# Kernel optimization log

Hardware: AMD Instinct MI355X
Metric: run time of the kernel (lower is better)

Reference implementation:

```python
import jax, jax.numpy as jnp
import numpy as np

B, S, H = 4, 2048, 512
DEPTH, EXP = 2, 4
MAX_LR = 0.1
C = 8            # n_chunks
L = S // C       # chunk length
HE = H * EXP


def _l2norm(x, eps=1e-12):
    n = jnp.sqrt(jnp.sum(x * x, axis=-1, keepdims=True))
    return x / jnp.maximum(n, eps)


def _mem_fwd(mw1, mb1, mw2, mb2, x):
    # ResLinear: residual MLP blocks, x <- x + W2 @ silu(W1 @ x + b1) + b2
    for d in range(DEPTH):
        h = jax.nn.silu(x @ mw1[d].T + mb1[d])
        x = x + h @ mw2[d].T + mb2[d]
    return x


def setup_inputs() -> dict:
    key = jax.random.key(0)
    ks = jax.random.split(key, 9)
    s = 1.0 / np.sqrt(H)
    s2 = 1.0 / np.sqrt(HE)
    return {
        "x": jax.random.normal(ks[0], (B, S, H), jnp.float32),
        "wq": jax.random.normal(ks[1], (H, H), jnp.float32) * s, "bq": jnp.zeros((H,), jnp.float32),
        "wk": jax.random.normal(ks[2], (H, H), jnp.float32) * s, "bk": jnp.zeros((H,), jnp.float32),
        "wv": jax.random.normal(ks[3], (H, H), jnp.float32) * s, "bv": jnp.zeros((H,), jnp.float32),
        "wlr": jax.random.normal(ks[4], (1, H), jnp.float32) * s, "blr": jnp.zeros((1,), jnp.float32),
        "wf": jax.random.normal(ks[5], (1, H), jnp.float32) * s, "bf": jnp.zeros((1,), jnp.float32),
        "wm": jax.random.normal(ks[6], (1, H), jnp.float32) * s, "bm": jnp.zeros((1,), jnp.float32),
        "mw1": jax.random.normal(ks[7], (DEPTH, HE, H), jnp.float32) * s,
        "mb1": jnp.zeros((DEPTH, HE), jnp.float32),
        "mw2": jax.random.normal(ks[8], (DEPTH, H, HE), jnp.float32) * s2,
        "mb2": jnp.zeros((DEPTH, H), jnp.float32),
        "mom_w1": jnp.zeros((DEPTH, HE, H), jnp.float32),
        "mom_b1": jnp.zeros((DEPTH, HE), jnp.float32),
        "mom_w2": jnp.zeros((DEPTH, H, HE), jnp.float32),
        "mom_b2": jnp.zeros((DEPTH, H), jnp.float32),
    }


def reference(x, wq, bq, wk, bk, wv, bv, wlr, blr, wf, bf, wm, bm,
              mw1, mb1, mw2, mb2, mom_w1, mom_b1, mom_w2, mom_b2):
    # projections (non-generating path; S % C == 0 so no padding)
    q = _l2norm(x @ wq.T + bq)                            # [B,S,H]
    k = _l2norm(x @ wk.T + bk).reshape(B, C, L, H)
    v = (x @ wv.T + bv).reshape(B, C, L, H)
    lr = jax.nn.sigmoid(x @ wlr.T + blr).reshape(B, C, L, 1) * MAX_LR
    forget = jax.nn.sigmoid(x @ wf.T + bf).reshape(B, C, L, 1)
    momg = jax.nn.sigmoid(x @ wm.T + bm).reshape(B, C, L, 1)

    mem = (mw1, mb1, mw2, mb2)

    def chunk_loss(mem_params, k_c, v_c, lr_c):
        # k_c,v_c: [B,L,H]; lr_c: [B,L,1]
        preds = _mem_fwd(*mem_params, k_c)
        loss = jnp.mean((preds - v_c) ** 2, axis=-1)      # [B,L]
        return jnp.sum(loss * lr_c[..., 0])

    # per-chunk synthetic gradients of the memory MLP, then mean over chunks
    grads = jax.vmap(jax.grad(chunk_loss), in_axes=(None, 1, 1, 1))(mem, k, v, lr)
    grads = jax.tree_util.tree_map(lambda g: jnp.mean(g, axis=0), grads)

    alpha = jnp.mean(forget, axis=(1, 2, 3))              # [B] forget gate
    theta = jnp.mean(lr, axis=(1, 2, 3))                  # [B] adaptive lr
    eta = jnp.mean(momg, axis=(1, 2, 3))                  # [B] momentum gate

    def update(p, g, m):
        shp = (B,) + (1,) * p.ndim
        a, t, e = alpha.reshape(shp), theta.reshape(shp), eta.reshape(shp)
        m_b = e * m[None] - t * g[None]                   # [B,*p.shape]
        return jnp.mean(p[None] * (1.0 - a) + m_b, axis=0)

    moms = (mom_w1, mom_b1, mom_w2, mom_b2)
    new_mem = tuple(update(p, g, m) for p, g, m in zip(mem, grads, moms))

    return _mem_fwd(*new_mem, q)                          # [B,S,H]
```

## Files before the change

### kernel.cpp

```cpp
#include <hip/hip_runtime.h>
#include <cstdint>
#include <cstddef>


#define NROWS 8192
#define HDIM  512
#define HEDIM 2048
#define NCHUNK 8
#define BK    64
#define DPCOEF (2.0f / (HDIM * NCHUNK))

typedef unsigned short u16;
typedef __attribute__((ext_vector_type(8))) unsigned short u16x8;
typedef __attribute__((ext_vector_type(8))) short bf16x8;
typedef __attribute__((ext_vector_type(4))) float f32x4;

__device__ __forceinline__ float sigmoidf_(float x){ return 1.0f/(1.0f+__expf(-x)); }
__device__ __forceinline__ float siluf_(float x){ return x*sigmoidf_(x); }
__device__ __forceinline__ float dsiluf_(float x){ float s=sigmoidf_(x); return s*(1.0f+x*(1.0f-s)); }
__device__ __forceinline__ u16 bf1_(float x){
    union{float f; unsigned u;} v; v.f = x;
    return (u16)((v.u + 0x7fffu + ((v.u>>16)&1u)) >> 16);
}
__device__ __forceinline__ float bf2f_(u16 h){
    union{unsigned u; float f;} v; v.u = ((unsigned)h) << 16; return v.f;
}
__device__ __forceinline__ int swkey_(int row){
    return (((row>>3)&1)<<2) | (((row>>4)&1)<<1) | ((row>>5)&1);
}
__device__ __forceinline__ void gl_lds16(const u16* g, u16* l){
    __builtin_amdgcn_global_load_lds(
        (const __attribute__((address_space(1))) unsigned*)g,
        (__attribute__((address_space(3))) unsigned*)l, 16, 0, 0);
}

template<int MODE, bool ATR>
__global__ __launch_bounds__(256)
void mgemm_k(const u16* __restrict__ A, const u16* __restrict__ B,
             const float* __restrict__ bias, const float* __restrict__ resF,
             const u16* __restrict__ resB, const u16* __restrict__ aux,
             const float* __restrict__ vf, const float* __restrict__ lrs,
             float* __restrict__ outF, u16* __restrict__ outB, u16* __restrict__ outB2,
             int M, int N, int K, int lda, int ldb)
{
    __shared__ __align__(128) u16 As[128*64];
    __shared__ __align__(128) u16 Bs[128*64];
    const int tid = threadIdx.x;
    const int lane = tid & 63, wvi = tid >> 6;
    const int wm = wvi >> 1, wn = wvi & 1;
    const int lr = lane & 15, lq = lane >> 4;
    const int m0 = blockIdx.y * 128, n0 = blockIdx.x * 128;

    int kbeg = 0, kend = K;
    if (MODE == 3){ const int ks = K >> 3; kbeg = blockIdx.z * ks; kend = kbeg + ks; }

    f32x4 acc[4][4];
    const f32x4 zz = {0.f,0.f,0.f,0.f};
    #pragma unroll
    for (int i = 0; i < 4; ++i)
        #pragma unroll
        for (int j = 0; j < 4; ++j) acc[i][j] = zz;

    int roffA[4], roffB[4];
    #pragma unroll
    for (int i = 0; i < 4; ++i){
        const int ra = wm*64 + i*16 + lr, rb = wn*64 + i*16 + lr;
        roffA[i] = ra*64 + ((lq ^ swkey_(ra)) << 3);
        roffB[i] = rb*64 + ((lq ^ swkey_(rb)) << 3);
    }

    for (int k0 = kbeg; k0 < kend; k0 += BK) {
        if (!ATR) {
            #pragma unroll
            for (int it = 0; it < 4; ++it){
                const int seg = it*4 + wvi;
                const int key = (((seg&1)<<2)|(((seg>>1)&1)<<1)|((seg>>2)&1));
                const int row = seg*8 + (lane>>3);
                const int chunk = (lane&7) ^ key;
                gl_lds16(A + (size_t)(m0+row)*lda + k0 + chunk*8, &As[seg*512]);
                gl_lds16(B + (size_t)(n0+row)*ldb + k0 + chunk*8, &Bs[seg*512]);
            }
        } else {
            #pragma unroll
            for (int r = 0; r < 2; ++r){
                const int slot = r*256 + tid;
                const int mc = slot & 15, kp = slot >> 4;
                const int chunk = kp >> 2, t = kp & 3;
                const int key = (((mc&1)<<2)|(((mc>>1)&1)<<1)|((mc>>2)&1));
                const int cs = ((chunk ^ key) << 3) + t*2;
                {
                    const u16* p = A + (size_t)(k0 + 2*kp) * lda + m0 + mc*8;
                    u16x8 e = *(const u16x8*)p;
                    u16x8 o = *(const u16x8*)(p + lda);
                    #pragma unroll
                    for (int j = 0; j < 8; ++j)
                        *(unsigned*)&As[(mc*8 + j)*64 + cs] = (unsigned)e[j] | ((unsigned)o[j] << 16);
                }
                {
                    const u16* p = B + (size_t)(k0 + 2*kp) * ldb + n0 + mc*8;
                    u16x8 e = *(const u16x8*)p;
                    u16x8 o = *(const u16x8*)(p + ldb);
                    #pragma unroll
                    for (int j = 0; j < 8; ++j)
                        *(unsigned*)&Bs[(mc*8 + j)*64 + cs] = (unsigned)e[j] | ((unsigned)o[j] << 16);
                }
            }
        }
        __syncthreads();
        #pragma unroll
        for (int ks = 0; ks < 2; ++ks) {
            bf16x8 afr[4], bfr[4];
            #pragma unroll
            for (int i = 0; i < 4; ++i){
                const int ra = wm*64 + i*16 + lr, rb = wn*64 + i*16 + lr;
                afr[i] = *(const bf16x8*)&As[ra*64 + (((ks*4 + lq) ^ swkey_(ra)) << 3)];
                bfr[i] = *(const bf16x8*)&Bs[rb*64 + (((ks*4 + lq) ^ swkey_(rb)) << 3)];
            }
            #pragma unroll
            for (int mi = 0; mi < 4; ++mi)
                #pragma unroll
                for (int ni = 0; ni < 4; ++ni)
                    acc[mi][ni] = __builtin_amdgcn_mfma_f32_16x16x32_bf16(afr[mi], bfr[ni], acc[mi][ni], 0, 0, 0);
        }
        __syncthreads();
    }
    (void)roffA; (void)roffB;

    #pragma unroll
    for (int ni = 0; ni < 4; ++ni){
        const int col = n0 + wn*64 + ni*16 + lr;
        float bv = 0.0f;
        if (MODE==0 || MODE==1 || MODE==2 || MODE==6 || MODE==7 || MODE==8 || MODE==9) bv = bias[col];
        #pragma unroll
        for (int mi = 0; mi < 4; ++mi){
            const int rbase = m0 + wm*64 + mi*16 + lq*4;
            #pragma unroll
            for (int v = 0; v < 4; ++v){
                const int row = rbase + v;
                const size_t idx = (size_t)row * N + col;
                const float o = acc[mi][ni][v];
                if (MODE == 0){ outF[idx] = o + bv; }
                else if (MODE == 1){
                    const float u = o + bv;
                    outB[idx]  = bf1_(siluf_(u));
                    outB2[idx] = bf1_(dsiluf_(u));
                }
                else if (MODE == 2){ outB[idx] = bf1_(siluf_(o + bv)); }
                else if (MODE == 3){ outF[(size_t)blockIdx.z * M * N + idx] = o; }
                else if (MODE == 4){ outB[idx] = bf1_(o * bf2f_(aux[idx])); }
                else if (MODE == 5){ outB[idx] = bf1_(o + resF[idx]); }
                else if (MODE == 6){ const float t = o + bv + resF[idx]; outF[idx] = t; outB[idx] = bf1_(t); }
                else if (MODE == 7){ outF[idx] = o + bv + resF[idx]; }
                else if (MODE == 8){
                    const float t = o + bv + bf2f_(resB[idx]);
                    const float g = lrs[row] * DPCOEF * (t - vf[idx]);
                    outF[idx] = g; outB[idx] = bf1_(g);
                }
                else if (MODE == 9){ outB[idx] = bf1_(o + bv + bf2f_(resB[idx])); }
            }
        }
    }
}

__global__ __launch_bounds__(256)
void cvt_k(const float* __restrict__ in, u16* __restrict__ out, int n8)
{
    const int i = blockIdx.x * 256 + threadIdx.x;
    if (i < n8){
        const float4 a = *(const float4*)(in + (size_t)i*8);
        const float4 b = *(const float4*)(in + (size_t)i*8 + 4);
        u16x8 o;
        o[0]=bf1_(a.x); o[1]=bf1_(a.y); o[2]=bf1_(a.z); o[3]=bf1_(a.w);
        o[4]=bf1_(b.x); o[5]=bf1_(b.y); o[6]=bf1_(b.z); o[7]=bf1_(b.w);
        *(u16x8*)(out + (size_t)i*8) = o;
    }
}

__global__ __launch_bounds__(256)
void tcvt_k(const float* __restrict__ in, u16* __restrict__ out, int R, int C)
{
    __shared__ float t[32][33];
    const int tx = threadIdx.x & 31, ty = threadIdx.x >> 5;
    const int c0 = blockIdx.x * 32, r0 = blockIdx.y * 32;
    #pragma unroll
    for (int j = 0; j < 4; ++j)
        t[ty + 8*j][tx] = in[(size_t)(r0 + ty + 8*j) * C + c0 + tx];
    __syncthreads();
    #pragma unroll
    for (int j = 0; j < 4; ++j)
        out[(size_t)(c0 + ty + 8*j) * R + r0 + tx] = bf1_(t[tx][ty + 8*j]);
}

template<bool WF32>
__global__ __launch_bounds__(64)
void l2norm_k(const float* __restrict__ in, float* __restrict__ outF, u16* __restrict__ outB)
{
    const float* p = in + (size_t)blockIdx.x * HDIM;
    const int t = threadIdx.x;
    float4 v0 = *(const float4*)(p + t*8), v1 = *(const float4*)(p + t*8 + 4);
    float s = v0.x*v0.x+v0.y*v0.y+v0.z*v0.z+v0.w*v0.w
            + v1.x*v1.x+v1.y*v1.y+v1.z*v1.z+v1.w*v1.w;
    #pragma unroll
    for (int o = 1; o < 64; o <<= 1) s += __shfl_xor(s, o);
    const float sc = 1.0f / fmaxf(sqrtf(s), 1e-12f);
    v0.x*=sc; v0.y*=sc; v0.z*=sc; v0.w*=sc;
    v1.x*=sc; v1.y*=sc; v1.z*=sc; v1.w*=sc;
    if (WF32){
        float* q = outF + (size_t)blockIdx.x * HDIM;
        *(float4*)(q + t*8) = v0; *(float4*)(q + t*8 + 4) = v1;
    }
    u16x8 ob;
    ob[0]=bf1_(v0.x); ob[1]=bf1_(v0.y); ob[2]=bf1_(v0.z); ob[3]=bf1_(v0.w);
    ob[4]=bf1_(v1.x); ob[5]=bf1_(v1.y); ob[6]=bf1_(v1.z); ob[7]=bf1_(v1.w);
    *(u16x8*)(outB + (size_t)blockIdx.x * HDIM + t*8) = ob;
}

__global__ __launch_bounds__(64)
void gates_k(const float* __restrict__ x,
             const float* __restrict__ wlr, const float* __restrict__ blr,
             const float* __restrict__ wf,  const float* __restrict__ bfp,
             const float* __restrict__ wm,  const float* __restrict__ bm,
             float* __restrict__ lr_s, float* __restrict__ f_s, float* __restrict__ m_s)
{
    const size_t row = blockIdx.x;
    const float* p = x + row * HDIM;
    const int t = threadIdx.x;
    float s0 = 0.f, s1 = 0.f, s2 = 0.f;
    #pragma unroll
    for (int i = 0; i < 8; i += 4){
        float4 xv = *(const float4*)(p   + t*8 + i);
        float4 a  = *(const float4*)(wlr + t*8 + i);
        float4 b  = *(const float4*)(wf  + t*8 + i);
        float4 c  = *(const float4*)(wm  + t*8 + i);
        s0 += xv.x*a.x + xv.y*a.y + xv.z*a.z + xv.w*a.w;
        s1 += xv.x*b.x + xv.y*b.y + xv.z*b.z + xv.w*b.w;
        s2 += xv.x*c.x + xv.y*c.y + xv.z*c.z + xv.w*c.w;
    }
    #pragma unroll
    for (int o = 1; o < 64; o <<= 1){
        s0 += __shfl_xor(s0, o); s1 += __shfl_xor(s1, o); s2 += __shfl_xor(s2, o);
    }
    if (t == 0){
        lr_s[row] = sigmoidf_(s0 + blr[0]) * 0.1f;
        f_s[row]  = sigmoidf_(s1 + bfp[0]);
        m_s[row]  = sigmoidf_(s2 + bm[0]);
    }
}

__global__ __launch_bounds__(256)
void scalars_k(const float* __restrict__ lr_s, const float* __restrict__ f_s,
               const float* __restrict__ m_s, float* __restrict__ sc)
{
    __shared__ float sh0[256], sh1[256], sh2[256];
    const int t = threadIdx.x;
    float s0 = 0.f, s1 = 0.f, s2 = 0.f;
    for (int i = t; i < NROWS; i += 256){ s0 += f_s[i]; s1 += lr_s[i]; s2 += m_s[i]; }
    sh0[t] = s0; sh1[t] = s1; sh2[t] = s2;
    __syncthreads();
    for (int o = 128; o > 0; o >>= 1){
        if (t < o){ sh0[t] += sh0[t+o]; sh1[t] += sh1[t+o]; sh2[t] += sh2[t+o]; }
        __syncthreads();
    }
    if (t == 0){
        sc[0] = sh0[0] / (float)NROWS;
        sc[1] = sh1[0] / (float)NROWS;
        sc[2] = sh2[0] / (float)NROWS;
    }
}

template<typename T>
__global__ __launch_bounds__(64)
void colsum_part_k(const T* __restrict__ g, float* __restrict__ part, int cols)
{
    const int c = blockIdx.x * 64 + threadIdx.x;
    const int rc = blockIdx.y;
    const T* p = g + (size_t)rc * 128 * cols + c;
    float s = 0.f;
    for (int r = 0; r < 128; ++r){
        if (sizeof(T) == 2) s += bf2f_(*(const u16*)(p + (size_t)r * cols));
        else                s += *(const float*)(p + (size_t)r * cols);
    }
    part[(size_t)rc * cols + c] = s;
}
__global__ __launch_bounds__(256)
void colsum_fin_k(const float* __restrict__ part, float* __restrict__ out, int cols)
{
    const int c = blockIdx.x * 256 + threadIdx.x;
    if (c < cols){
        float s = 0.f;
        for (int r = 0; r < 64; ++r) s += part[(size_t)r * cols + c];
        out[c] = s;
    }
}

__global__ __launch_bounds__(256)
void update_k(const float* __restrict__ p, const float* __restrict__ g,
              const float* __restrict__ mom, const float* __restrict__ sc,
              float* __restrict__ np_, int n)
{
    const int i = blockIdx.x * 256 + threadIdx.x;
    if (i < n) np_[i] = p[i] * (1.0f - sc[0]) + sc[2] * mom[i] - sc[1] * g[i];
}

__global__ __launch_bounds__(256)
void fupdate8_k(const float* __restrict__ p, const float* __restrict__ P,
                const float* __restrict__ mom, const float* __restrict__ sc,
                u16* __restrict__ nWb, int n)
{
    const int i = blockIdx.x * 256 + threadIdx.x;
    if (i < n){
        float g = 0.f;
        #pragma unroll
        for (int z = 0; z < 8; ++z) g += P[(size_t)z * n + i];
        nWb[i] = bf1_(p[i] * (1.0f - sc[0]) + sc[2] * mom[i] - sc[1] * g);
    }
}

extern "C" void kernel_launch(void* const* d_in, const int* in_sizes, int n_in,
                              void* d_out, int out_size, void* d_ws, size_t ws_size,
                              hipStream_t stream)
{
    const float* x      = (const float*)d_in[0];
    const float* wq     = (const float*)d_in[1];
    const float* bq     = (const float*)d_in[2];
    const float* wk     = (const float*)d_in[3];
    const float* bk     = (const float*)d_in[4];
    const float* wv     = (const float*)d_in[5];
    const float* bv     = (const float*)d_in[6];
    const float* wlr    = (const float*)d_in[7];
    const float* blr    = (const float*)d_in[8];
    const float* wf     = (const float*)d_in[9];
    const float* bfp    = (const float*)d_in[10];
    const float* wm     = (const float*)d_in[11];
    const float* bm     = (const float*)d_in[12];
    const float* mw1    = (const float*)d_in[13];
    const float* mb1    = (const float*)d_in[14];
    const float* mw2    = (const float*)d_in[15];
    const float* mb2    = (const float*)d_in[16];
    const float* mom_w1 = (const float*)d_in[17];
    const float* mom_b1 = (const float*)d_in[18];
    const float* mom_w2 = (const float*)d_in[19];
    const float* mom_b2 = (const float*)d_in[20];
    float* out = (float*)d_out;

    char* base = (char*)d_ws;
    size_t off = 0;
    auto alloc = [&](size_t bytes)->char*{ char* p = base + off; off += (bytes + 255) & ~(size_t)255; return p; };
    const size_t NHf  = (size_t)NROWS * HDIM  * 4;
    const size_t NHb  = (size_t)NROWS * HDIM  * 2;
    const size_t NHEb = (size_t)NROWS * HEDIM * 2;
    const int    WHALF = HEDIM * HDIM;

    float* F1   = (float*)alloc(NHf);
    float* F2   = (float*)alloc(NHf);
    u16*  xb    = (u16*) alloc(NHb);
    u16*  kb    = (u16*) alloc(NHb);
    u16*  x1b   = (u16*) alloc(NHb);
    u16*  g2b   = (u16*) alloc(NHb);
    u16*  hb    = (u16*) alloc(NHEb);
    u16*  db    = (u16*) alloc(NHEb);
    u16*  dhb   = (u16*) alloc(NHEb);
    u16*  wqb   = (u16*) alloc((size_t)HDIM*HDIM*2);
    u16*  wkb   = (u16*) alloc((size_t)HDIM*HDIM*2);
    u16*  wvb   = (u16*) alloc((size_t)HDIM*HDIM*2);
    u16*  mw1b  = (u16*) alloc((size_t)2*WHALF*2);
    u16*  mw2b  = (u16*) alloc((size_t)2*WHALF*2);
    u16*  mw2Tb = (u16*) alloc((size_t)2*WHALF*2);
    u16*  mw1T1b= (u16*) alloc((size_t)WHALF*2);
    u16*  nW1b  = (u16*) alloc((size_t)2*WHALF*2);
    u16*  nW2b  = (u16*) alloc((size_t)2*WHALF*2);
    float* cpart= (float*)alloc((size_t)64*HEDIM*4);
    float* lr_s = (float*)alloc((size_t)NROWS*4);
    float* f_s  = (float*)alloc((size_t)NROWS*4);
    float* m_s  = (float*)alloc((size_t)NROWS*4);
    float* sc   = (float*)alloc(64);
    float* gb1  = (float*)alloc((size_t)2*HEDIM*4);
    float* gb2  = (float*)alloc((size_t)2*HDIM*4);
    float* nb1  = (float*)alloc((size_t)2*HEDIM*4);
    float* nb2  = (float*)alloc((size_t)2*HDIM*4);
    u16* qb  = xb;
    u16* g1b = g2b;
    float* P = (float*)db;

    const dim3 blk(256);
    const dim3 gN512 (HDIM/128,  NROWS/128);
    const dim3 gN2048(HEDIM/128, NROWS/128);
    const dim3 gTN2  (HEDIM/128, HDIM/128, 8);
    const dim3 gTN1  (HDIM/128,  HEDIM/128, 8);

    const float* mw1_1 = mw1 + (size_t)WHALF;
    const float* mw2_1 = mw2 + (size_t)WHALF;

    #define GARG(Ab,Bb,bi,rF,rB,ax,vv,ll,oF,oB,oB2,M,N,K,la,lb) \
        ((const u16*)(Ab),(const u16*)(Bb),(const float*)(bi),(const float*)(rF),\
         (const u16*)(rB),(const u16*)(ax),(const float*)(vv),(const float*)(ll),\
         (float*)(oF),(u16*)(oB),(u16*)(oB2),(M),(N),(K),(la),(lb))

    cvt_k<<<dim3((NROWS*HDIM/8)/256), blk, 0, stream>>>(x, xb, NROWS*HDIM/8);
    cvt_k<<<dim3((HDIM*HDIM/8)/256), blk, 0, stream>>>(wq, wqb, HDIM*HDIM/8);
    cvt_k<<<dim3((HDIM*HDIM/8)/256), blk, 0, stream>>>(wk, wkb, HDIM*HDIM/8);
    cvt_k<<<dim3((HDIM*HDIM/8)/256), blk, 0, stream>>>(wv, wvb, HDIM*HDIM/8);
    cvt_k<<<dim3((2*WHALF/8)/256), blk, 0, stream>>>(mw1, mw1b, 2*WHALF/8);
    cvt_k<<<dim3((2*WHALF/8)/256), blk, 0, stream>>>(mw2, mw2b, 2*WHALF/8);
    tcvt_k<<<dim3(HEDIM/32, HDIM/32), blk, 0, stream>>>(mw2,   mw2Tb,         HDIM, HEDIM);
    tcvt_k<<<dim3(HEDIM/32, HDIM/32), blk, 0, stream>>>(mw2_1, mw2Tb + WHALF, HDIM, HEDIM);
    tcvt_k<<<dim3(HDIM/32, HEDIM/32), blk, 0, stream>>>(mw1_1, mw1T1b,        HEDIM, HDIM);
    gates_k<<<NROWS, 64, 0, stream>>>(x, wlr, blr, wf, bfp, wm, bm, lr_s, f_s, m_s);
    scalars_k<<<1, blk, 0, stream>>>(lr_s, f_s, m_s, sc);

    mgemm_k<0,false><<<gN512, blk, 0, stream>>>GARG(xb, wkb, bk, 0,0,0,0,0, F1, 0,0, NROWS,HDIM,HDIM, HDIM,HDIM);
    l2norm_k<false><<<NROWS, 64, 0, stream>>>(F1, nullptr, kb);
    mgemm_k<0,false><<<gN512, blk, 0, stream>>>GARG(xb, wvb, bv, 0,0,0,0,0, F2, 0,0, NROWS,HDIM,HDIM, HDIM,HDIM);

    mgemm_k<2,false><<<gN2048, blk, 0, stream>>>GARG(kb, mw1b, mb1, 0,0,0,0,0, 0, hb, 0, NROWS,HEDIM,HDIM, HDIM,HDIM);
    mgemm_k<9,false><<<gN512, blk, 0, stream>>>GARG(hb, mw2b, mb2, 0, kb, 0,0,0, 0, x1b, 0, NROWS,HDIM,HEDIM, HEDIM,HEDIM);
    mgemm_k<1,false><<<gN2048, blk, 0, stream>>>GARG(x1b, mw1b+WHALF, mb1+HEDIM, 0,0,0,0,0, 0, hb, db, NROWS,HEDIM,HDIM, HDIM,HDIM);
    mgemm_k<8,false><<<gN512, blk, 0, stream>>>GARG(hb, mw2b+WHALF, mb2+HDIM, 0, x1b, 0, F2, lr_s, out, g2b, 0, NROWS,HDIM,HEDIM, HEDIM,HEDIM);

    colsum_part_k<float><<<dim3(HDIM/64,64), 64, 0, stream>>>(out, cpart, HDIM);
    colsum_fin_k<<<dim3(HDIM/256), blk, 0, stream>>>(cpart, gb2 + HDIM, HDIM);
    update_k<<<dim3(HDIM/256), blk, 0, stream>>>(mb2+HDIM, gb2+HDIM, mom_b2+HDIM, sc, nb2+HDIM, HDIM);
    mgemm_k<4,false><<<gN2048, blk, 0, stream>>>GARG(g2b, mw2Tb+WHALF, 0,0,0, db, 0,0, 0, dhb, 0, NROWS,HEDIM,HDIM, HDIM,HDIM);
    mgemm_k<3,true><<<gTN2, blk, 0, stream>>>GARG(g2b, hb, 0,0,0,0,0,0, P, 0,0, HDIM,HEDIM,NROWS, HDIM,HEDIM);
    fupdate8_k<<<dim3(WHALF/256), blk, 0, stream>>>(mw2_1, P, mom_w2+WHALF, sc, nW2b+WHALF, WHALF);
    colsum_part_k<u16><<<dim3(HEDIM/64,64), 64, 0, stream>>>(dhb, cpart, HEDIM);
    colsum_fin_k<<<dim3(HEDIM/256), blk, 0, stream>>>(cpart, gb1 + HEDIM, HEDIM);
    update_k<<<dim3(HEDIM/256), blk, 0, stream>>>(mb1+HEDIM, gb1+HEDIM, mom_b1+HEDIM, sc, nb1+HEDIM, HEDIM);
    mgemm_k<3,true><<<gTN1, blk, 0, stream>>>GARG(dhb, x1b, 0,0,0,0,0,0, P, 0,0, HEDIM,HDIM,NROWS, HEDIM,HDIM);
    fupdate8_k<<<dim3(WHALF/256), blk, 0, stream>>>(mw1_1, P, mom_w1+WHALF, sc, nW1b+WHALF, WHALF);
    mgemm_k<5,false><<<gN512, blk, 0, stream>>>GARG(dhb, mw1T1b, 0, out, 0,0,0,0, 0, g1b, 0, NROWS,HDIM,HEDIM, HEDIM,HEDIM);

    colsum_part_k<u16><<<dim3(HDIM/64,64), 64, 0, stream>>>(g1b, cpart, HDIM);
    colsum_fin_k<<<dim3(HDIM/256), blk, 0, stream>>>(cpart, gb2, HDIM);
    update_k<<<dim3(HDIM/256), blk, 0, stream>>>(mb2, gb2, mom_b2, sc, nb2, HDIM);
    mgemm_k<1,false><<<gN2048, blk, 0, stream>>>GARG(kb, mw1b, mb1, 0,0,0,0,0, 0, hb, db, NROWS,HEDIM,HDIM, HDIM,HDIM);
    mgemm_k<4,false><<<gN2048, blk, 0, stream>>>GARG(g1b, mw2Tb, 0,0,0, db, 0,0, 0, dhb, 0, NROWS,HEDIM,HDIM, HDIM,HDIM);
    mgemm_k<3,true><<<gTN2, blk, 0, stream>>>GARG(g1b, hb, 0,0,0,0,0,0, P, 0,0, HDIM,HEDIM,NROWS, HDIM,HEDIM);
    fupdate8_k<<<dim3(WHALF/256), blk, 0, stream>>>(mw2, P, mom_w2, sc, nW2b, WHALF);
    colsum_part_k<u16><<<dim3(HEDIM/64,64), 64, 0, stream>>>(dhb, cpart, HEDIM);
    colsum_fin_k<<<dim3(HEDIM/256), blk, 0, stream>>>(cpart, gb1, HEDIM);
    update_k<<<dim3(HEDIM/256), blk, 0, stream>>>(mb1, gb1, mom_b1, sc, nb1, HEDIM);
    mgemm_k<3,true><<<gTN1, blk, 0, stream>>>GARG(dhb, kb, 0,0,0,0,0,0, P, 0,0, HEDIM,HDIM,NROWS, HEDIM,HDIM);
    fupdate8_k<<<dim3(WHALF/256), blk, 0, stream>>>(mw1, P, mom_w1, sc, nW1b, WHALF);

    mgemm_k<0,false><<<gN512, blk, 0, stream>>>GARG(xb, wqb, bq, 0,0,0,0,0, F2, 0,0, NROWS,HDIM,HDIM, HDIM,HDIM);
    l2norm_k<true><<<NROWS, 64, 0, stream>>>(F2, F2, qb);
    mgemm_k<2,false><<<gN2048, blk, 0, stream>>>GARG(qb, nW1b, nb1, 0,0,0,0,0, 0, hb, 0, NROWS,HEDIM,HDIM, HDIM,HDIM);
    mgemm_k<6,false><<<gN512, blk, 0, stream>>>GARG(hb, nW2b, nb2, F2, 0,0,0,0, F1, x1b, 0, NROWS,HDIM,HEDIM, HEDIM,HEDIM);
    mgemm_k<2,false><<<gN2048, blk, 0, stream>>>GARG(x1b, nW1b+WHALF, nb1+HEDIM, 0,0,0,0,0, 0, hb, 0, NROWS,HEDIM,HDIM, HDIM,HDIM);
    mgemm_k<7,false><<<gN512, blk, 0, stream>>>GARG(hb, nW2b+WHALF, nb2+HDIM, F1, 0,0,0,0, out, 0,0, NROWS,HDIM,HEDIM, HEDIM,HEDIM);

    #undef GARG
    (void)in_sizes; (void)n_in; (void)out_size; (void)ws_size;
}
```

Baseline: 838.5 us.

## Fuse KVQ projections, remap GEMM blocks, split-K 16 with bf16 partials, merge small kernels

Merges the K, V and Q projections into one GEMM over a concatenated weight matrix, with strided l2norm and MODE 8 reads. Remaps block IDs so neighbouring workgroups are spread across XCDs. Raises the weight-gradient split-K from 8 to 16 and stores the partials in bf16 to cut traffic. Fuses the column-sum finalize with the bias update and removes dead offset code. This cuts kernel launches and memory traffic, at the cost of some precision in the gradient partial sums.

```diff
diff --git a/kernel.cpp b/kernel.cpp
--- a/kernel.cpp
+++ b/kernel.cpp
@@ -41,7 +41,7 @@
              const u16* __restrict__ resB, const u16* __restrict__ aux,
              const float* __restrict__ vf, const float* __restrict__ lrs,
              float* __restrict__ outF, u16* __restrict__ outB, u16* __restrict__ outB2,
-             int M, int N, int K, int lda, int ldb)
+             int M, int N, int K, int lda, int ldb, int ldv)
 {
     __shared__ __align__(128) u16 As[128*64];
     __shared__ __align__(128) u16 Bs[128*64];
@@ -49,10 +49,15 @@
     const int lane = tid & 63, wvi = tid >> 6;
     const int wm = wvi >> 1, wn = wvi & 1;
     const int lr = lane & 15, lq = lane >> 4;
-    const int m0 = blockIdx.y * 128, n0 = blockIdx.x * 128;
+
+    const int gx = gridDim.x;
+    const int nwg = gx * gridDim.y;
+    int bid = blockIdx.y * gx + blockIdx.x;
+    bid = (bid & 7) * (nwg >> 3) + (bid >> 3);
+    const int m0 = (bid / gx) * 128, n0 = (bid % gx) * 128;
 
     int kbeg = 0, kend = K;
-    if (MODE == 3){ const int ks = K >> 3; kbeg = blockIdx.z * ks; kend = kbeg + ks; }
+    if (MODE == 3){ const int ks = K >> 4; kbeg = blockIdx.z * ks; kend = kbeg + ks; }
 
     f32x4 acc[4][4];
     const f32x4 zz = {0.f,0.f,0.f,0.f};
@@ -60,14 +65,6 @@
     for (int i = 0; i < 4; ++i)
         #pragma unroll
         for (int j = 0; j < 4; ++j) acc[i][j] = zz;
-
-    int roffA[4], roffB[4];
-    #pragma unroll
-    for (int i = 0; i < 4; ++i){
-        const int ra = wm*64 + i*16 + lr, rb = wn*64 + i*16 + lr;
-        roffA[i] = ra*64 + ((lq ^ swkey_(ra)) << 3);
-        roffB[i] = rb*64 + ((lq ^ swkey_(rb)) << 3);
-    }
 
     for (int k0 = kbeg; k0 < kend; k0 += BK) {
         if (!ATR) {
@@ -124,7 +121,6 @@
         }
         __syncthreads();
     }
-    (void)roffA; (void)roffB;
 
     #pragma unroll
     for (int ni = 0; ni < 4; ++ni){
@@ -146,14 +142,14 @@
                     outB2[idx] = bf1_(dsiluf_(u));
                 }
                 else if (MODE == 2){ outB[idx] = bf1_(siluf_(o + bv)); }
-                else if (MODE == 3){ outF[(size_t)blockIdx.z * M * N + idx] = o; }
+                else if (MODE == 3){ outB[(size_t)blockIdx.z * M * N + idx] = bf1_(o); }
                 else if (MODE == 4){ outB[idx] = bf1_(o * bf2f_(aux[idx])); }
                 else if (MODE == 5){ outB[idx] = bf1_(o + resF[idx]); }
                 else if (MODE == 6){ const float t = o + bv + resF[idx]; outF[idx] = t; outB[idx] = bf1_(t); }
                 else if (MODE == 7){ outF[idx] = o + bv + resF[idx]; }
                 else if (MODE == 8){
                     const float t = o + bv + bf2f_(resB[idx]);
-                    const float g = lrs[row] * DPCOEF * (t - vf[idx]);
+                    const float g = lrs[row] * DPCOEF * (t - vf[(size_t)row * ldv + col]);
                     outF[idx] = g; outB[idx] = bf1_(g);
                 }
                 else if (MODE == 9){ outB[idx] = bf1_(o + bv + bf2f_(resB[idx])); }
@@ -177,6 +173,30 @@
 }
 
 __global__ __launch_bounds__(256)
+void prep_kvq_k(const float* __restrict__ wk, const float* __restrict__ wv,
+                const float* __restrict__ wq, const float* __restrict__ bk,
+                const float* __restrict__ bv, const float* __restrict__ bq,
+                u16* __restrict__ wkvqb, float* __restrict__ bkvq)
+{
+    const int per = HDIM*HDIM/8;
+    const int id = blockIdx.x * 256 + threadIdx.x;
+    if (id < 3*per){
+        const float* src = (id < per) ? wk : (id < 2*per ? wv : wq);
+        const int i = id - (id < per ? 0 : (id < 2*per ? per : 2*per));
+        const float4 a = *(const float4*)(src + (size_t)i*8);
+        const float4 b = *(const float4*)(src + (size_t)i*8 + 4);
+        u16x8 o;
+        o[0]=bf1_(a.x); o[1]=bf1_(a.y); o[2]=bf1_(a.z); o[3]=bf1_(a.w);
+        o[4]=bf1_(b.x); o[5]=bf1_(b.y); o[6]=bf1_(b.z); o[7]=bf1_(b.w);
+        *(u16x8*)(wkvqb + (size_t)id*8) = o;
+    } else {
+        const int j = id - 3*per;
+        if (j < 3*HDIM)
+            bkvq[j] = (j < HDIM) ? bk[j] : (j < 2*HDIM ? bv[j-HDIM] : bq[j-2*HDIM]);
+    }
+}
+
+__global__ __launch_bounds__(256)
 void tcvt_k(const float* __restrict__ in, u16* __restrict__ out, int R, int C)
 {
     __shared__ float t[32][33];
@@ -193,9 +213,10 @@
 
 template<bool WF32>
 __global__ __launch_bounds__(64)
-void l2norm_k(const float* __restrict__ in, float* __restrict__ outF, u16* __restrict__ outB)
-{
-    const float* p = in + (size_t)blockIdx.x * HDIM;
+void l2norm_k(const float* __restrict__ in, int ld,
+              float* __restrict__ outF, u16* __restrict__ outB)
+{
+    const float* p = in + (size_t)blockIdx.x * ld;
     const int t = threadIdx.x;
     float4 v0 = *(const float4*)(p + t*8), v1 = *(const float4*)(p + t*8 + 4);
     float s = v0.x*v0.x+v0.y*v0.y+v0.z*v0.z+v0.w*v0.w
@@ -282,36 +303,30 @@
     }
     part[(size_t)rc * cols + c] = s;
 }
-__global__ __launch_bounds__(256)
-void colsum_fin_k(const float* __restrict__ part, float* __restrict__ out, int cols)
+
+__global__ __launch_bounds__(256)
+void colsum_upd_k(const float* __restrict__ part, const float* __restrict__ p,
+                  const float* __restrict__ mom, const float* __restrict__ sc,
+                  float* __restrict__ nb, int cols)
 {
     const int c = blockIdx.x * 256 + threadIdx.x;
     if (c < cols){
         float s = 0.f;
         for (int r = 0; r < 64; ++r) s += part[(size_t)r * cols + c];
-        out[c] = s;
-    }
-}
-
-__global__ __launch_bounds__(256)
-void update_k(const float* __restrict__ p, const float* __restrict__ g,
-              const float* __restrict__ mom, const float* __restrict__ sc,
-              float* __restrict__ np_, int n)
-{
-    const int i = blockIdx.x * 256 + threadIdx.x;
-    if (i < n) np_[i] = p[i] * (1.0f - sc[0]) + sc[2] * mom[i] - sc[1] * g[i];
-}
-
-__global__ __launch_bounds__(256)
-void fupdate8_k(const float* __restrict__ p, const float* __restrict__ P,
-                const float* __restrict__ mom, const float* __restrict__ sc,
-                u16* __restrict__ nWb, int n)
+        nb[c] = p[c] * (1.0f - sc[0]) + sc[2] * mom[c] - sc[1] * s;
+    }
+}
+
+__global__ __launch_bounds__(256)
+void fupdate16_k(const float* __restrict__ p, const u16* __restrict__ P,
+                 const float* __restrict__ mom, const float* __restrict__ sc,
+                 u16* __restrict__ nWb, int n)
 {
     const int i = blockIdx.x * 256 + threadIdx.x;
     if (i < n){
         float g = 0.f;
         #pragma unroll
-        for (int z = 0; z < 8; ++z) g += P[(size_t)z * n + i];
+        for (int z = 0; z < 16; ++z) g += bf2f_(P[(size_t)z * n + i]);
         nWb[i] = bf1_(p[i] * (1.0f - sc[0]) + sc[2] * mom[i] - sc[1] * g);
     }
 }
@@ -351,7 +366,6 @@
     const size_t NHEb = (size_t)NROWS * HEDIM * 2;
     const int    WHALF = HEDIM * HDIM;
 
-    float* F1   = (float*)alloc(NHf);
     float* F2   = (float*)alloc(NHf);
     u16*  xb    = (u16*) alloc(NHb);
     u16*  kb    = (u16*) alloc(NHb);
@@ -359,10 +373,9 @@
     u16*  g2b   = (u16*) alloc(NHb);
     u16*  hb    = (u16*) alloc(NHEb);
     u16*  db    = (u16*) alloc(NHEb);
-    u16*  dhb   = (u16*) alloc(NHEb);
-    u16*  wqb   = (u16*) alloc((size_t)HDIM*HDIM*2);
-    u16*  wkb   = (u16*) alloc((size_t)HDIM*HDIM*2);
-    u16*  wvb   = (u16*) alloc((size_t)HDIM*HDIM*2);
+    u16*  dhb   = (u16*) alloc(NHEb + NHf);
+    u16*  wkvqb = (u16*) alloc((size_t)3*HDIM*HDIM*2);
+    float* bkvq = (float*)alloc((size_t)3*HDIM*4);
     u16*  mw1b  = (u16*) alloc((size_t)2*WHALF*2);
     u16*  mw2b  = (u16*) alloc((size_t)2*WHALF*2);
     u16*  mw2Tb = (u16*) alloc((size_t)2*WHALF*2);
@@ -374,32 +387,31 @@
     float* f_s  = (float*)alloc((size_t)NROWS*4);
     float* m_s  = (float*)alloc((size_t)NROWS*4);
     float* sc   = (float*)alloc(64);
-    float* gb1  = (float*)alloc((size_t)2*HEDIM*4);
-    float* gb2  = (float*)alloc((size_t)2*HDIM*4);
     float* nb1  = (float*)alloc((size_t)2*HEDIM*4);
     float* nb2  = (float*)alloc((size_t)2*HDIM*4);
     u16* qb  = xb;
     u16* g1b = g2b;
-    float* P = (float*)db;
+    float* P3 = (float*)dhb;
+    float* F1 = (float*)((char*)dhb + NHEb);
+    u16*  Pp  = db;
 
     const dim3 blk(256);
+    const dim3 gKVQ (3*HDIM/128, NROWS/128);
     const dim3 gN512 (HDIM/128,  NROWS/128);
     const dim3 gN2048(HEDIM/128, NROWS/128);
-    const dim3 gTN2  (HEDIM/128, HDIM/128, 8);
-    const dim3 gTN1  (HDIM/128,  HEDIM/128, 8);
+    const dim3 gTN2  (HEDIM/128, HDIM/128, 16);
+    const dim3 gTN1  (HDIM/128,  HEDIM/128, 16);
 
     const float* mw1_1 = mw1 + (size_t)WHALF;
     const float* mw2_1 = mw2 + (size_t)WHALF;
 
-    #define GARG(Ab,Bb,bi,rF,rB,ax,vv,ll,oF,oB,oB2,M,N,K,la,lb) \
+    #define GARG(Ab,Bb,bi,rF,rB,ax,vv,ll,oF,oB,oB2,M,N,K,la,lb,lv) \
         ((const u16*)(Ab),(const u16*)(Bb),(const float*)(bi),(const float*)(rF),\
          (const u16*)(rB),(const u16*)(ax),(const float*)(vv),(const float*)(ll),\
-         (float*)(oF),(u16*)(oB),(u16*)(oB2),(M),(N),(K),(la),(lb))
+         (float*)(oF),(u16*)(oB),(u16*)(oB2),(M),(N),(K),(la),(lb),(lv))
 
     cvt_k<<<dim3((NROWS*HDIM/8)/256), blk, 0, stream>>>(x, xb, NROWS*HDIM/8);
-    cvt_k<<<dim3((HDIM*HDIM/8)/256), blk, 0, stream>>>(wq, wqb, HDIM*HDIM/8);
-    cvt_k<<<dim3((HDIM*HDIM/8)/256), blk, 0, stream>>>(wk, wkb, HDIM*HDIM/8);
-    cvt_k<<<dim3((HDIM*HDIM/8)/256), blk, 0, stream>>>(wv, wvb, HDIM*HDIM/8);
+    prep_kvq_k<<<dim3((3*HDIM*HDIM/8 + 3*HDIM + 255)/256), blk, 0, stream>>>(wk, wv, wq, bk, bv, bq, wkvqb, bkvq);
     cvt_k<<<dim3((2*WHALF/8)/256), blk, 0, stream>>>(mw1, mw1b, 2*WHALF/8);
     cvt_k<<<dim3((2*WHALF/8)/256), blk, 0, stream>>>(mw2, mw2b, 2*WHALF/8);
     tcvt_k<<<dim3(HEDIM/32, HDIM/32), blk, 0, stream>>>(mw2,   mw2Tb,         HDIM, HEDIM);
@@ -408,47 +420,41 @@
     gates_k<<<NROWS, 64, 0, stream>>>(x, wlr, blr, wf, bfp, wm, bm, lr_s, f_s, m_s);
     scalars_k<<<1, blk, 0, stream>>>(lr_s, f_s, m_s, sc);
 
-    mgemm_k<0,false><<<gN512, blk, 0, stream>>>GARG(xb, wkb, bk, 0,0,0,0,0, F1, 0,0, NROWS,HDIM,HDIM, HDIM,HDIM);
-    l2norm_k<false><<<NROWS, 64, 0, stream>>>(F1, nullptr, kb);
-    mgemm_k<0,false><<<gN512, blk, 0, stream>>>GARG(xb, wvb, bv, 0,0,0,0,0, F2, 0,0, NROWS,HDIM,HDIM, HDIM,HDIM);
-
-    mgemm_k<2,false><<<gN2048, blk, 0, stream>>>GARG(kb, mw1b, mb1, 0,0,0,0,0, 0, hb, 0, NROWS,HEDIM,HDIM, HDIM,HDIM);
-    mgemm_k<9,false><<<gN512, blk, 0, stream>>>GARG(hb, mw2b, mb2, 0, kb, 0,0,0, 0, x1b, 0, NROWS,HDIM,HEDIM, HEDIM,HEDIM);
-    mgemm_k<1,false><<<gN2048, blk, 0, stream>>>GARG(x1b, mw1b+WHALF, mb1+HEDIM, 0,0,0,0,0, 0, hb, db, NROWS,HEDIM,HDIM, HDIM,HDIM);
-    mgemm_k<8,false><<<gN512, blk, 0, stream>>>GARG(hb, mw2b+WHALF, mb2+HDIM, 0, x1b, 0, F2, lr_s, out, g2b, 0, NROWS,HDIM,HEDIM, HEDIM,HEDIM);
+    mgemm_k<0,false><<<gKVQ, blk, 0, stream>>>GARG(xb, wkvqb, bkvq, 0,0,0,0,0, P3, 0,0, NROWS,3*HDIM,HDIM, HDIM,HDIM, 3*HDIM);
+    l2norm_k<false><<<NROWS, 64, 0, stream>>>(P3,          3*HDIM, nullptr, kb);
+    l2norm_k<true ><<<NROWS, 64, 0, stream>>>(P3 + 2*HDIM, 3*HDIM, F2, qb);
+
+    mgemm_k<2,false><<<gN2048, blk, 0, stream>>>GARG(kb, mw1b, mb1, 0,0,0,0,0, 0, hb, 0, NROWS,HEDIM,HDIM, HDIM,HDIM, HEDIM);
+    mgemm_k<9,false><<<gN512, blk, 0, stream>>>GARG(hb, mw2b, mb2, 0, kb, 0,0,0, 0, x1b, 0, NROWS,HDIM,HEDIM, HEDIM,HEDIM, HDIM);
+    mgemm_k<1,false><<<gN2048, blk, 0, stream>>>GARG(x1b, mw1b+WHALF, mb1+HEDIM, 0,0,0,0,0, 0, hb, db, NROWS,HEDIM,HDIM, HDIM,HDIM, HEDIM);
+    mgemm_k<8,false><<<gN512, blk, 0, stream>>>GARG(hb, mw2b+WHALF, mb2+HDIM, 0, x1b, 0, P3 + HDIM, lr_s, out, g2b, 0, NROWS,HDIM,HEDIM, HEDIM,HEDIM, 3*HDIM);
 
     colsum_part_k<float><<<dim3(HDIM/64,64), 64, 0, stream>>>(out, cpart, HDIM);
-    colsum_fin_k<<<dim3(HDIM/256), blk, 0, stream>>>(cpart, gb2 + HDIM, HDIM);
-    update_k<<<dim3(HDIM/256), blk, 0, stream>>>(mb2+HDIM, gb2+HDIM, mom_b2+HDIM, sc, nb2+HDIM, HDIM);
-    mgemm_k<4,false><<<gN2048, blk, 0, stream>>>GARG(g2b, mw2Tb+WHALF, 0,0,0, db, 0,0, 0, dhb, 0, NROWS,HEDIM,HDIM, HDIM,HDIM);
-    mgemm_k<3,true><<<gTN2, blk, 0, stream>>>GARG(g2b, hb, 0,0,0,0,0,0, P, 0,0, HDIM,HEDIM,NROWS, HDIM,HEDIM);
-    fupdate8_k<<<dim3(WHALF/256), blk, 0, stream>>>(mw2_1, P, mom_w2+WHALF, sc, nW2b+WHALF, WHALF);
+    colsum_upd_k<<<dim3(HDIM/256), blk, 0, stream>>>(cpart, mb2+HDIM, mom_b2+HDIM, sc, nb2+HDIM, HDIM);
+    mgemm_k<4,false><<<gN2048, blk, 0, stream>>>GARG(g2b, mw2Tb+WHALF, 0,0,0, db, 0,0, 0, dhb, 0, NROWS,HEDIM,HDIM, HDIM,HDIM, HEDIM);
+    mgemm_k<3,true><<<gTN2, blk, 0, stream>>>GARG(g2b, hb, 0,0,0,0,0,0, 0, Pp, 0, HDIM,HEDIM,NROWS, HDIM,HEDIM, HEDIM);
+    fupdate16_k<<<dim3(WHALF/256), blk, 0, stream>>>(mw2_1, Pp, mom_w2+WHALF, sc, nW2b+WHALF, WHALF);
     colsum_part_k<u16><<<dim3(HEDIM/64,64), 64, 0, stream>>>(dhb, cpart, HEDIM);
-    colsum_fin_k<<<dim3(HEDIM/256), blk, 0, stream>>>(cpart, gb1 + HEDIM, HEDIM);
-    update_k<<<dim3(HEDIM/256), blk, 0, stream>>>(mb1+HEDIM, gb1+HEDIM, mom_b1+HEDIM, sc, nb1+HEDIM, HEDIM);
-    mgemm_k<3,true><<<gTN1, blk, 0, stream>>>GARG(dhb, x1b, 0,0,0,0,0,0, P, 0,0, HEDIM,HDIM,NROWS, HEDIM,HDIM);
-    fupdate8_k<<<dim3(WHALF/256), blk, 0, stream>>>(mw1_1, P, mom_w1+WHALF, sc, nW1b+WHALF, WHALF);
-    mgemm_k<5,false><<<gN512, blk, 0, stream>>>GARG(dhb, mw1T1b, 0, out, 0,0,0,0, 0, g1b, 0, NROWS,HDIM,HEDIM, HEDIM,HEDIM);
+    colsum_upd_k<<<dim3(HEDIM/256), blk, 0, stream>>>(cpart, mb1+HEDIM, mom_b1+HEDIM, sc, nb1+HEDIM, HEDIM);
+    mgemm_k<3,true><<<gTN1, blk, 0, stream>>>GARG(dhb, x1b, 0,0,0,0,0,0, 0, Pp, 0, HEDIM,HDIM,NROWS, HEDIM,HDIM, HDIM);
+    fupdate16_k<<<dim3(WHALF/256), blk, 0, stream>>>(mw1_1, Pp, mom_w1+WHALF, sc, nW1b+WHALF, WHALF);
+    mgemm_k<5,false><<<gN512, blk, 0, stream>>>GARG(dhb, mw1T1b, 0, out, 0,0,0,0, 0, g1b, 0, NROWS,HDIM,HEDIM, HEDIM,HEDIM, HDIM);
 
     colsum_part_k<u16><<<dim3(HDIM/64,64), 64, 0, stream>>>(g1b, cpart, HDIM);
-    colsum_fin_k<<<dim3(HDIM/256), blk, 0, stream>>>(cpart, gb2, HDIM);
-    update_k<<<dim3(HDIM/256), blk, 0, stream>>>(mb2, gb2, mom_b2, sc, nb2, HDIM);
-    mgemm_k<1,false><<<gN2048, blk, 0, stream>>>GARG(kb, mw1b, mb1, 0,0,0,0,0, 0, hb, db, NROWS,HEDIM,HDIM, HDIM,HDIM);
-    mgemm_k<4,false><<<gN2048, blk, 0, stream>>>GARG(g1b, mw2Tb, 0,0,0, db, 0,0, 0, dhb, 0, NROWS,HEDIM,HDIM, HDIM,HDIM);
-    mgemm_k<3,true><<<gTN2, blk, 0, stream>>>GARG(g1b, hb, 0,0,0,0,0,0, P, 0,0, HDIM,HEDIM,NROWS, HDIM,HEDIM);
-    fupdate8_k<<<dim3(WHALF/256), blk, 0, stream>>>(mw2, P, mom_w2, sc, nW2b, WHALF);
+    colsum_upd_k<<<dim3(HDIM/256), blk, 0, stream>>>(cpart, mb2, mom_b2, sc, nb2, HDIM);
+    mgemm_k<1,false><<<gN2048, blk, 0, stream>>>GARG(kb, mw1b, mb1, 0,0,0,0,0, 0, hb, db, NROWS,HEDIM,HDIM, HDIM,HDIM, HEDIM);
+    mgemm_k<4,false><<<gN2048, blk, 0, stream>>>GARG(g1b, mw2Tb, 0,0,0, db, 0,0, 0, dhb, 0, NROWS,HEDIM,HDIM, HDIM,HDIM, HEDIM);
+    mgemm_k<3,true><<<gTN2, blk, 0, stream>>>GARG(g1b, hb, 0,0,0,0,0,0, 0, Pp, 0, HDIM,HEDIM,NROWS, HDIM,HEDIM, HEDIM);
+    fupdate16_k<<<dim3(WHALF/256), blk, 0, stream>>>(mw2, Pp, mom_w2, sc, nW2b, WHALF);
     colsum_part_k<u16><<<dim3(HEDIM/64,64), 64, 0, stream>>>(dhb, cpart, HEDIM);
-    colsum_fin_k<<<dim3(HEDIM/256), blk, 0, stream>>>(cpart, gb1, HEDIM);
-    update_k<<<dim3(HEDIM/256), blk, 0, stream>>>(mb1, gb1, mom_b1, sc, nb1, HEDIM);
-    mgemm_k<3,true><<<gTN1, blk, 0, stream>>>GARG(dhb, kb, 0,0,0,0,0,0, P, 0,0, HEDIM,HDIM,NROWS, HEDIM,HDIM);
-    fupdate8_k<<<dim3(WHALF/256), blk, 0, stream>>>(mw1, P, mom_w1, sc, nW1b, WHALF);
-
-    mgemm_k<0,false><<<gN512, blk, 0, stream>>>GARG(xb, wqb, bq, 0,0,0,0,0, F2, 0,0, NROWS,HDIM,HDIM, HDIM,HDIM);
-    l2norm_k<true><<<NROWS, 64, 0, stream>>>(F2, F2, qb);
-    mgemm_k<2,false><<<gN2048, blk, 0, stream>>>GARG(qb, nW1b, nb1, 0,0,0,0,0, 0, hb, 0, NROWS,HEDIM,HDIM, HDIM,HDIM);
-    mgemm_k<6,false><<<gN512, blk, 0, stream>>>GARG(hb, nW2b, nb2, F2, 0,0,0,0, F1, x1b, 0, NROWS,HDIM,HEDIM, HEDIM,HEDIM);
-    mgemm_k<2,false><<<gN2048, blk, 0, stream>>>GARG(x1b, nW1b+WHALF, nb1+HEDIM, 0,0,0,0,0, 0, hb, 0, NROWS,HEDIM,HDIM, HDIM,HDIM);
-    mgemm_k<7,false><<<gN512, blk, 0, stream>>>GARG(hb, nW2b+WHALF, nb2+HDIM, F1, 0,0,0,0, out, 0,0, NROWS,HDIM,HEDIM, HEDIM,HEDIM);
+    colsum_upd_k<<<dim3(HEDIM/256), blk, 0, stream>>>(cpart, mb1, mom_b1, sc, nb1, HEDIM);
+    mgemm_k<3,true><<<gTN1, blk, 0, stream>>>GARG(dhb, kb, 0,0,0,0,0,0, 0, Pp, 0, HEDIM,HDIM,NROWS, HEDIM,HDIM, HDIM);
+    fupdate16_k<<<dim3(WHALF/256), blk, 0, stream>>>(mw1, Pp, mom_w1, sc, nW1b, WHALF);
+
+    mgemm_k<2,false><<<gN2048, blk, 0, stream>>>GARG(qb, nW1b, nb1, 0,0,0,0,0, 0, hb, 0, NROWS,HEDIM,HDIM, HDIM,HDIM, HEDIM);
+    mgemm_k<6,false><<<gN512, blk, 0, stream>>>GARG(hb, nW2b, nb2, F2, 0,0,0,0, F1, x1b, 0, NROWS,HDIM,HEDIM, HEDIM,HEDIM, HDIM);
+    mgemm_k<2,false><<<gN2048, blk, 0, stream>>>GARG(x1b, nW1b+WHALF, nb1+HEDIM, 0,0,0,0,0, 0, hb, 0, NROWS,HEDIM,HDIM, HDIM,HDIM, HEDIM);
+    mgemm_k<7,false><<<gN512, blk, 0, stream>>>GARG(hb, nW2b+WHALF, nb2+HDIM, F1, 0,0,0,0, out, 0,0, NROWS,HDIM,HEDIM, HEDIM,HEDIM, HDIM);
 
     #undef GARG
     (void)in_sizes; (void)n_in; (void)out_size; (void)ws_size;
```

New measurement: 807.7 us. -3.7%, faster.
